# Kernel tuning notes

Measured on AMD Instinct MI355X. Metric: run time of the kernel, lower is better.

## Reference

```python
import jax, jax.numpy as jnp
import numpy as np

M_SQRT1_2 = 0.7071067811865476
P_DROP = 0.1  # activation_dropout


def setup_inputs() -> dict:
    key = jax.random.key(0)
    k1, k2, k3, k4 = jax.random.split(key, 4)
    N, FFN, EMB = 8192, 4096, 1024
    x = jax.random.normal(k1, (N, FFN), dtype=jnp.float16)
    weight = (jax.random.normal(k2, (EMB, FFN), dtype=jnp.float32) * (1.0 / np.sqrt(FFN))).astype(jnp.float16)
    bias = jax.random.normal(k3, (EMB,), dtype=jnp.float16)
    mask = jax.random.uniform(k4, (N, FFN)) >= P_DROP  # keep mask (bool)
    return {"x": x, "weight": weight, "bias": bias, "mask": mask}


def reference(x, weight, bias, mask):
    # GELU computed in fp32, cast back to fp16 (matches the custom IR)
    xf = x.astype(jnp.float32)
    g = (0.5 * xf * (1.0 + jax.lax.erf(xf * M_SQRT1_2))).astype(jnp.float16)
    # dropout: mask then scale by 1/(1-p) in fp16
    scale = jnp.float16(1.0 / (1.0 - P_DROP))
    h = g * mask.astype(jnp.float16) * scale  # [N, FFN]
    # y[N0, N2] = sum_N1 h[N0, N1] * weight[N2, N1] + bias[N2]
    y = jnp.einsum('nf,ef->ne', h, weight) + bias[None, :]
    return y
```

## Files before the change

kernel.cpp:

```cpp
#include <hip/hip_runtime.h>
#include <stdint.h>

typedef uint32_t u32;
typedef uint16_t u16;

static constexpr int M_DIM = 8192;
static constexpr int N_DIM = 1024;
static constexpr int K_DIM = 4096;

static constexpr int BM = 256;
static constexpr int BN = 128;
static constexpr int BK = 64;
static constexpr int KT64 = K_DIM / BK;
static constexpr int K_TILES32 = K_DIM / 32;
static constexpr int MB_TILES = M_DIM / 16;
static constexpr int NB_TILES = N_DIM / 16;

static constexpr size_t FRAG_U16 = 512;
static constexpr size_t HT_BYTES = (size_t)MB_TILES * K_TILES32 * FRAG_U16 * 2;
static constexpr size_t WT_BYTES = (size_t)NB_TILES * K_TILES32 * FRAG_U16 * 2;
static constexpr size_t WS_NEEDED = HT_BYTES + WT_BYTES;

typedef __attribute__((ext_vector_type(8))) _Float16 half8;
typedef __attribute__((ext_vector_type(4))) float f32x4;

__device__ __forceinline__ u32 pack2(float a, float b) {
  union { _Float16 h[2]; u32 u; } p;
  p.h[0] = (_Float16)a;
  p.h[1] = (_Float16)b;
  return p.u;
}

__device__ __forceinline__ float gelu_drop(float x, u32 keep) {
  float ax = fabsf(x);
  float z  = ax * 0.70710678f;
  float t  = __builtin_amdgcn_rcpf(fmaf(0.3275911f, z, 1.0f));
  float poly = fmaf(fmaf(fmaf(fmaf(1.061405429f, t, -1.453152027f),
                              t, 1.421413741f),
                         t, -0.284496736f),
                    t, 0.254829592f) * t;
  float e   = exp2f(z * z * -1.44269504f);
  float erf = fmaf(-poly, e, 1.0f);
  float g   = 0.5f * x * (1.0f + copysignf(erf, x));
  return keep ? g * 1.1111112f : 0.0f;
}

__device__ __forceinline__ void async_cp16(const void* g, void* l) {
  __builtin_amdgcn_global_load_lds((__attribute__((address_space(1))) u32*)g,
                                   (__attribute__((address_space(3))) u32*)l,
                                   16, 0, 0);
}

static constexpr int H_WAVES = MB_TILES * K_TILES32;
static constexpr int W_WAVES = NB_TILES * K_TILES32;
static constexpr int PACK_BLOCKS = (H_WAVES + W_WAVES) / 4;

__global__ __launch_bounds__(256)
void pack_kernel(const float* __restrict__ X, const int* __restrict__ Mask,
                 const float* __restrict__ W, u16* __restrict__ Ht, u16* __restrict__ Wt) {
  const int l     = threadIdx.x & 63;
  const int fi    = blockIdx.x * 4 + (threadIdx.x >> 6);
  const int row16 = l & 15;
  const int kof   = (l >> 4) << 3;

  if (fi < H_WAVES) {
    const int mb = fi >> 7, kt = fi & 127;
    const float* xp = X    + (size_t)(mb * 16 + row16) * K_DIM + kt * 32 + kof;
    const int*   mp = Mask + (size_t)(mb * 16 + row16) * K_DIM + kt * 32 + kof;
    float4 x0 = *(const float4*)(xp + 0);
    float4 x1 = *(const float4*)(xp + 4);
    uint4  m0 = *(const uint4*)(mp + 0);
    uint4  m1 = *(const uint4*)(mp + 4);
    u32 o0 = pack2(gelu_drop(x0.x, m0.x), gelu_drop(x0.y, m0.y));
    u32 o1 = pack2(gelu_drop(x0.z, m0.z), gelu_drop(x0.w, m0.w));
    u32 o2 = pack2(gelu_drop(x1.x, m1.x), gelu_drop(x1.y, m1.y));
    u32 o3 = pack2(gelu_drop(x1.z, m1.z), gelu_drop(x1.w, m1.w));
    *(uint4*)(Ht + (size_t)fi * FRAG_U16 + l * 8) = make_uint4(o0, o1, o2, o3);
  } else {
    const int fj = fi - H_WAVES;
    const int nb = fj >> 7, kt = fj & 127;
    const float* wp = W + (size_t)(nb * 16 + row16) * K_DIM + kt * 32 + kof;
    float4 w0 = *(const float4*)(wp + 0);
    float4 w1 = *(const float4*)(wp + 4);
    *(uint4*)(Wt + (size_t)fj * FRAG_U16 + l * 8) =
        make_uint4(pack2(w0.x, w0.y), pack2(w0.z, w0.w), pack2(w1.x, w1.y), pack2(w1.z, w1.w));
  }
}

__global__ __launch_bounds__(512, 1)
void gemm_kernel(const u16* __restrict__ Ht, const u16* __restrict__ Wt,
                 const float* __restrict__ Bias, float* __restrict__ Out) {
  __shared__ __attribute__((aligned(16))) u16 Abuf[2][BM * BK];
  __shared__ __attribute__((aligned(16))) u16 Bbuf[2][BN * BK];

  const int tid  = threadIdx.x;
  const int lane = tid & 63;
  const int wv   = tid >> 6;
  const int wr   = wv >> 1;
  const int wc   = wv & 1;

  const int bm = blockIdx.x & 31;
  const int bn = blockIdx.x >> 5;
  const int m0 = bm * BM;
  const int n0 = bn * BN;

  const char* aG = (const char*)Ht;
  const char* bG = (const char*)Wt;
  size_t aOff[4], bOff[2];
#pragma unroll
  for (int p = 0; p < 4; ++p) {
    const int s = tid + 512 * p, f = s >> 6;
    aOff[p] = ((size_t)(bm * 16 + (f >> 1)) * K_TILES32 + (f & 1)) * 1024 + (size_t)(s & 63) * 16;
  }
#pragma unroll
  for (int p = 0; p < 2; ++p) {
    const int s = tid + 512 * p, f = s >> 6;
    bOff[p] = ((size_t)(bn * 8 + (f >> 1)) * K_TILES32 + (f & 1)) * 1024 + (size_t)(s & 63) * 16;
  }

  auto stage = [&](int kt, int buf) {
    const size_t ko = (size_t)kt * 2048;
    char* ad = (char*)Abuf[buf];
    char* bd = (char*)Bbuf[buf];
#pragma unroll
    for (int p = 0; p < 4; ++p)
      async_cp16(aG + aOff[p] + ko, ad + (tid + 512 * p) * 16);
#pragma unroll
    for (int p = 0; p < 2; ++p)
      async_cp16(bG + bOff[p] + ko, bd + (tid + 512 * p) * 16);
  };

  f32x4 acc[4][4];
#pragma unroll
  for (int i = 0; i < 4; ++i)
#pragma unroll
    for (int j = 0; j < 4; ++j)
      acc[i][j] = (f32x4){0.f, 0.f, 0.f, 0.f};

  auto compute = [&](int buf) {
    const char* ab = (const char*)Abuf[buf];
    const char* bb = (const char*)Bbuf[buf];
#pragma unroll
    for (int kk = 0; kk < 2; ++kk) {
      half8 ar[4], br[4];
#pragma unroll
      for (int i = 0; i < 4; ++i)
        ar[i] = *(const half8*)(ab + (((wr * 4 + i) * 2 + kk) * 64 + lane) * 16);
#pragma unroll
      for (int j = 0; j < 4; ++j)
        br[j] = *(const half8*)(bb + (((wc * 4 + j) * 2 + kk) * 64 + lane) * 16);
#pragma unroll
      for (int i = 0; i < 4; ++i)
#pragma unroll
        for (int j = 0; j < 4; ++j)
          acc[i][j] = __builtin_amdgcn_mfma_f32_16x16x32_f16(ar[i], br[j], acc[i][j], 0, 0, 0);
    }
  };

  stage(0, 0);
  __syncthreads();

#pragma unroll 1
  for (int kt = 0; kt < KT64; kt += 2) {
    if (kt + 1 < KT64) stage(kt + 1, 1);
    compute(0);
    __syncthreads();
    if (kt + 2 < KT64) stage(kt + 2, 0);
    compute(1);
    __syncthreads();
  }

  const int fr = lane & 15;
  const int rq = (lane >> 4) << 2;
  float bv[4];
#pragma unroll
  for (int j = 0; j < 4; ++j)
    bv[j] = Bias[n0 + wc * 64 + j * 16 + fr];

#pragma unroll
  for (int i = 0; i < 4; ++i) {
    const int row0 = m0 + wr * 64 + i * 16 + rq;
#pragma unroll
    for (int j = 0; j < 4; ++j) {
      const int col = n0 + wc * 64 + j * 16 + fr;
#pragma unroll
      for (int r = 0; r < 4; ++r)
        Out[(size_t)(row0 + r) * N_DIM + col] = acc[i][j][r] + bv[j];
    }
  }
}

static constexpr int A_STRIDE = 40;

__global__ __launch_bounds__(256, 2)
void fused_fallback_kernel(const float* __restrict__ X, const float* __restrict__ W,
                           const float* __restrict__ Bias, const int* __restrict__ Mask,
                           float* __restrict__ Out) {
  __shared__ __attribute__((aligned(16))) _Float16 As[128 * A_STRIDE];
  __shared__ __attribute__((aligned(16))) _Float16 Bs[128 * 32];

  const int tid  = threadIdx.x;
  const int lane = tid & 63;
  const int wv   = tid >> 6;
  const int wr   = wv >> 1;
  const int wc   = wv & 1;
  const int bm = blockIdx.x & 63;
  const int bn = blockIdx.x >> 6;
  const int m0 = bm * 128;
  const int n0 = bn * 128;

  const int a_m = tid >> 1;
  const int a_k = (tid & 1) << 4;
  const float* xptr = X    + (size_t)(m0 + a_m) * K_DIM + a_k;
  const int*   mptr = Mask + (size_t)(m0 + a_m) * K_DIM + a_k;
  _Float16* a_lds = &As[a_m * A_STRIDE + a_k];

  const int i0 = tid, i1 = tid + 256;
  const float* wp0 = W + (size_t)(n0 + (i0 >> 2)) * K_DIM + ((i0 & 3) << 3);
  const float* wp1 = W + (size_t)(n0 + (i1 >> 2)) * K_DIM + ((i1 & 3) << 3);
  _Float16* bl0 = &Bs[i0 * 8];
  _Float16* bl1 = &Bs[i1 * 8];

  f32x4 acc[4][4];
#pragma unroll
  for (int i = 0; i < 4; ++i)
#pragma unroll
    for (int j = 0; j < 4; ++j)
      acc[i][j] = (f32x4){0.f, 0.f, 0.f, 0.f};

  float4 xf0 = *(const float4*)(xptr +  0);
  float4 xf1 = *(const float4*)(xptr +  4);
  float4 xf2 = *(const float4*)(xptr +  8);
  float4 xf3 = *(const float4*)(xptr + 12);
  uint4  mr0 = *(const uint4*)(mptr +  0);
  uint4  mr1 = *(const uint4*)(mptr +  4);
  uint4  mr2 = *(const uint4*)(mptr +  8);
  uint4  mr3 = *(const uint4*)(mptr + 12);
  float4 wf0 = *(const float4*)(wp0 + 0);
  float4 wf1 = *(const float4*)(wp0 + 4);
  float4 wf2 = *(const float4*)(wp1 + 0);
  float4 wf3 = *(const float4*)(wp1 + 4);

#pragma unroll 1
  for (int kt = 0; kt < 128; ++kt) {
    {
      float xs[16] = {xf0.x, xf0.y, xf0.z, xf0.w, xf1.x, xf1.y, xf1.z, xf1.w,
                      xf2.x, xf2.y, xf2.z, xf2.w, xf3.x, xf3.y, xf3.z, xf3.w};
      u32 mk[16]   = {mr0.x, mr0.y, mr0.z, mr0.w, mr1.x, mr1.y, mr1.z, mr1.w,
                      mr2.x, mr2.y, mr2.z, mr2.w, mr3.x, mr3.y, mr3.z, mr3.w};
      u32 ow[8];
#pragma unroll
      for (int e = 0; e < 8; ++e)
        ow[e] = pack2(gelu_drop(xs[2 * e], mk[2 * e]), gelu_drop(xs[2 * e + 1], mk[2 * e + 1]));
      ((uint4*)a_lds)[0] = make_uint4(ow[0], ow[1], ow[2], ow[3]);
      ((uint4*)a_lds)[1] = make_uint4(ow[4], ow[5], ow[6], ow[7]);
    }
    {
      *(uint4*)bl0 = make_uint4(pack2(wf0.x, wf0.y), pack2(wf0.z, wf0.w),
                                pack2(wf1.x, wf1.y), pack2(wf1.z, wf1.w));
      *(uint4*)bl1 = make_uint4(pack2(wf2.x, wf2.y), pack2(wf2.z, wf2.w),
                                pack2(wf3.x, wf3.y), pack2(wf3.z, wf3.w));
    }
    __syncthreads();

    if (kt + 1 < 128) {
      xptr += 32; mptr += 32; wp0 += 32; wp1 += 32;
      xf0 = *(const float4*)(xptr +  0);
      xf1 = *(const float4*)(xptr +  4);
      xf2 = *(const float4*)(xptr +  8);
      xf3 = *(const float4*)(xptr + 12);
      mr0 = *(const uint4*)(mptr +  0);
      mr1 = *(const uint4*)(mptr +  4);
      mr2 = *(const uint4*)(mptr +  8);
      mr3 = *(const uint4*)(mptr + 12);
      wf0 = *(const float4*)(wp0 + 0);
      wf1 = *(const float4*)(wp0 + 4);
      wf2 = *(const float4*)(wp1 + 0);
      wf3 = *(const float4*)(wp1 + 4);
    }

    {
      const int fr2 = lane & 15;
      const int fk2 = (lane >> 4) << 3;
      half8 ar[4], br[4];
#pragma unroll
      for (int i = 0; i < 4; ++i)
        ar[i] = *(const half8*)&As[(wr * 64 + i * 16 + fr2) * A_STRIDE + fk2];
#pragma unroll
      for (int j = 0; j < 4; ++j)
        br[j] = *(const half8*)&Bs[(wc * 64 + j * 16 + fr2) * 32 + fk2];
#pragma unroll
      for (int i = 0; i < 4; ++i)
#pragma unroll
        for (int j = 0; j < 4; ++j)
          acc[i][j] = __builtin_amdgcn_mfma_f32_16x16x32_f16(ar[i], br[j], acc[i][j], 0, 0, 0);
    }
    __syncthreads();
  }

  const int fr = lane & 15;
  const int rq = (lane >> 4) << 2;
  float bv[4];
#pragma unroll
  for (int j = 0; j < 4; ++j)
    bv[j] = Bias[n0 + wc * 64 + j * 16 + fr];
#pragma unroll
  for (int i = 0; i < 4; ++i) {
    const int row0 = m0 + wr * 64 + i * 16 + rq;
#pragma unroll
    for (int j = 0; j < 4; ++j) {
      const int col = n0 + wc * 64 + j * 16 + fr;
#pragma unroll
      for (int r = 0; r < 4; ++r)
        Out[(size_t)(row0 + r) * N_DIM + col] = acc[i][j][r] + bv[j];
    }
  }
}

extern "C" void kernel_launch(void* const* d_in, const int* in_sizes, int n_in,
                              void* d_out, int out_size, void* d_ws, size_t ws_size,
                              hipStream_t stream) {
  const float* X    = (const float*)d_in[0];
  const float* W    = (const float*)d_in[1];
  const float* Bias = (const float*)d_in[2];
  const int*   Mk   = (const int*)d_in[3];
  float* Out = (float*)d_out;

  if (ws_size >= WS_NEEDED) {
    u16* Ht = (u16*)d_ws;
    u16* Wt = (u16*)((char*)d_ws + HT_BYTES);
    pack_kernel<<<PACK_BLOCKS, 256, 0, stream>>>(X, Mk, W, Ht, Wt);
    gemm_kernel<<<(M_DIM / BM) * (N_DIM / BN), 512, 0, stream>>>(Ht, Wt, Bias, Out);
  } else {
    fused_fallback_kernel<<<64 * 8, 256, 0, stream>>>(X, W, Bias, Mk, Out);
  }
}
```

Baseline: 392.5 us.

## Triple-buffer GEMM LDS with vmcnt waits and widen pack to two fragments per wave

The GEMM main loop moves from double to triple LDS buffering. Loads are issued two K-tiles ahead, and each iteration uses one barrier guarded by a partial s_waitcnt vmcnt in place of __syncthreads. This is meant to hide global-to-LDS latency behind MFMA, and s_setprio raises wave priority around the MFMA bursts. The pack kernel now handles 16 contiguous K elements per lane, covering two fragments, so each lane issues wider loads and two stores. The cost is more LDS (three buffers of 48KB each, 144KB), and correctness depends on the hardcoded vmcnt(6) matching the number of loads per stage.

After: 401.2 us. 2.2% more time.

```diff
diff --git a/kernel.cpp b/kernel.cpp
--- a/kernel.cpp
+++ b/kernel.cpp
@@ -51,47 +51,68 @@
                                    16, 0, 0);
 }
 
-static constexpr int H_WAVES = MB_TILES * K_TILES32;
-static constexpr int W_WAVES = NB_TILES * K_TILES32;
-static constexpr int PACK_BLOCKS = (H_WAVES + W_WAVES) / 4;
+static constexpr int H_PAIRS = MB_TILES * (K_TILES32 / 2);
+static constexpr int W_PAIRS = NB_TILES * (K_TILES32 / 2);
+static constexpr int PACK_BLOCKS = (H_PAIRS + W_PAIRS) / 4;
 
 __global__ __launch_bounds__(256)
 void pack_kernel(const float* __restrict__ X, const int* __restrict__ Mask,
                  const float* __restrict__ W, u16* __restrict__ Ht, u16* __restrict__ Wt) {
   const int l     = threadIdx.x & 63;
-  const int fi    = blockIdx.x * 4 + (threadIdx.x >> 6);
+  const int pi    = blockIdx.x * 4 + (threadIdx.x >> 6);
   const int row16 = l & 15;
-  const int kof   = (l >> 4) << 3;
-
-  if (fi < H_WAVES) {
-    const int mb = fi >> 7, kt = fi & 127;
-    const float* xp = X    + (size_t)(mb * 16 + row16) * K_DIM + kt * 32 + kof;
-    const int*   mp = Mask + (size_t)(mb * 16 + row16) * K_DIM + kt * 32 + kof;
+  const int kof   = (l >> 4) << 4;
+
+  const int fsub = kof >> 5;
+  const int q0   = (kof & 31) >> 3;
+
+  if (pi < H_PAIRS) {
+    const int mb = pi >> 6, kp = pi & 63;
+    const size_t src = (size_t)(mb * 16 + row16) * K_DIM + kp * 64 + kof;
+    const float* xp = X    + src;
+    const int*   mp = Mask + src;
     float4 x0 = *(const float4*)(xp + 0);
     float4 x1 = *(const float4*)(xp + 4);
+    float4 x2 = *(const float4*)(xp + 8);
+    float4 x3 = *(const float4*)(xp + 12);
     uint4  m0 = *(const uint4*)(mp + 0);
     uint4  m1 = *(const uint4*)(mp + 4);
+    uint4  m2 = *(const uint4*)(mp + 8);
+    uint4  m3 = *(const uint4*)(mp + 12);
     u32 o0 = pack2(gelu_drop(x0.x, m0.x), gelu_drop(x0.y, m0.y));
     u32 o1 = pack2(gelu_drop(x0.z, m0.z), gelu_drop(x0.w, m0.w));
     u32 o2 = pack2(gelu_drop(x1.x, m1.x), gelu_drop(x1.y, m1.y));
     u32 o3 = pack2(gelu_drop(x1.z, m1.z), gelu_drop(x1.w, m1.w));
-    *(uint4*)(Ht + (size_t)fi * FRAG_U16 + l * 8) = make_uint4(o0, o1, o2, o3);
+    u32 o4 = pack2(gelu_drop(x2.x, m2.x), gelu_drop(x2.y, m2.y));
+    u32 o5 = pack2(gelu_drop(x2.z, m2.z), gelu_drop(x2.w, m2.w));
+    u32 o6 = pack2(gelu_drop(x3.x, m3.x), gelu_drop(x3.y, m3.y));
+    u32 o7 = pack2(gelu_drop(x3.z, m3.z), gelu_drop(x3.w, m3.w));
+    const int f = kp * 2 + fsub;
+    u16* dst = Ht + (size_t)(mb * 128 + f) * FRAG_U16 + (size_t)(row16 + 16 * q0) * 8;
+    *(uint4*)(dst)       = make_uint4(o0, o1, o2, o3);
+    *(uint4*)(dst + 128) = make_uint4(o4, o5, o6, o7);
   } else {
-    const int fj = fi - H_WAVES;
-    const int nb = fj >> 7, kt = fj & 127;
-    const float* wp = W + (size_t)(nb * 16 + row16) * K_DIM + kt * 32 + kof;
+    const int pj = pi - H_PAIRS;
+    const int nb = pj >> 6, kp = pj & 63;
+    const float* wp = W + (size_t)(nb * 16 + row16) * K_DIM + kp * 64 + kof;
     float4 w0 = *(const float4*)(wp + 0);
     float4 w1 = *(const float4*)(wp + 4);
-    *(uint4*)(Wt + (size_t)fj * FRAG_U16 + l * 8) =
-        make_uint4(pack2(w0.x, w0.y), pack2(w0.z, w0.w), pack2(w1.x, w1.y), pack2(w1.z, w1.w));
+    float4 w2 = *(const float4*)(wp + 8);
+    float4 w3 = *(const float4*)(wp + 12);
+    const int f = kp * 2 + fsub;
+    u16* dst = Wt + (size_t)(nb * 128 + f) * FRAG_U16 + (size_t)(row16 + 16 * q0) * 8;
+    *(uint4*)(dst)       = make_uint4(pack2(w0.x, w0.y), pack2(w0.z, w0.w),
+                                      pack2(w1.x, w1.y), pack2(w1.z, w1.w));
+    *(uint4*)(dst + 128) = make_uint4(pack2(w2.x, w2.y), pack2(w2.z, w2.w),
+                                      pack2(w3.x, w3.y), pack2(w3.z, w3.w));
   }
 }
 
 __global__ __launch_bounds__(512, 1)
 void gemm_kernel(const u16* __restrict__ Ht, const u16* __restrict__ Wt,
                  const float* __restrict__ Bias, float* __restrict__ Out) {
-  __shared__ __attribute__((aligned(16))) u16 Abuf[2][BM * BK];
-  __shared__ __attribute__((aligned(16))) u16 Bbuf[2][BN * BK];
+  __shared__ __attribute__((aligned(16))) u16 Abuf[3][BM * BK];
+  __shared__ __attribute__((aligned(16))) u16 Bbuf[3][BN * BK];
 
   const int tid  = threadIdx.x;
   const int lane = tid & 63;
@@ -149,25 +170,38 @@
 #pragma unroll
       for (int j = 0; j < 4; ++j)
         br[j] = *(const half8*)(bb + (((wc * 4 + j) * 2 + kk) * 64 + lane) * 16);
+      __builtin_amdgcn_s_setprio(1);
 #pragma unroll
       for (int i = 0; i < 4; ++i)
 #pragma unroll
         for (int j = 0; j < 4; ++j)
           acc[i][j] = __builtin_amdgcn_mfma_f32_16x16x32_f16(ar[i], br[j], acc[i][j], 0, 0, 0);
+      __builtin_amdgcn_s_setprio(0);
     }
   };
 
   stage(0, 0);
-  __syncthreads();
-
+  stage(1, 1);
+
+  int cur = 0;
 #pragma unroll 1
-  for (int kt = 0; kt < KT64; kt += 2) {
-    if (kt + 1 < KT64) stage(kt + 1, 1);
-    compute(0);
-    __syncthreads();
-    if (kt + 2 < KT64) stage(kt + 2, 0);
-    compute(1);
-    __syncthreads();
+  for (int kt = 0; kt < KT64; ++kt) {
+    if (kt + 2 < KT64) {
+      asm volatile("s_waitcnt vmcnt(6)" ::: "memory");
+      __builtin_amdgcn_s_barrier();
+      asm volatile("" ::: "memory");
+      stage(kt + 2, cur == 0 ? 2 : cur - 1);
+    } else if (kt + 1 < KT64) {
+      asm volatile("s_waitcnt vmcnt(6)" ::: "memory");
+      __builtin_amdgcn_s_barrier();
+      asm volatile("" ::: "memory");
+    } else {
+      asm volatile("s_waitcnt vmcnt(0)" ::: "memory");
+      __builtin_amdgcn_s_barrier();
+      asm volatile("" ::: "memory");
+    }
+    compute(cur);
+    cur = (cur == 2) ? 0 : cur + 1;
   }
 
   const int fr = lane & 15;
```

## Use row-major H with XOR-swizzled LDS, smaller 128x128 tiles, streaming pack

Applied to the files above, without the earlier changes.

The GELU/dropout pack now writes H row-major with fully coalesced 16-element-per-thread streaming loads, software-pipelined across four iterations, instead of fragment-tiled. W is still packed in MFMA fragment order. The GEMM moves from 256x128 tiles with 512 threads and a double-buffered LDS to 128x128 tiles with 256 threads, two blocks per CU and a single LDS buffer. A tiles are read from LDS through an XOR swizzle to avoid bank conflicts. Dropping the double buffer exposes load latency, which the second resident block is expected to hide.

After: 416.3 us. 1.06x slower.

```diff
diff --git a/kernel.cpp b/kernel.cpp
--- a/kernel.cpp
+++ b/kernel.cpp
@@ -8,18 +8,10 @@
 static constexpr int N_DIM = 1024;
 static constexpr int K_DIM = 4096;
 
-static constexpr int BM = 256;
-static constexpr int BN = 128;
-static constexpr int BK = 64;
-static constexpr int KT64 = K_DIM / BK;
-static constexpr int K_TILES32 = K_DIM / 32;
-static constexpr int MB_TILES = M_DIM / 16;
-static constexpr int NB_TILES = N_DIM / 16;
-
+static constexpr size_t H_BYTES  = (size_t)M_DIM * K_DIM * 2;
 static constexpr size_t FRAG_U16 = 512;
-static constexpr size_t HT_BYTES = (size_t)MB_TILES * K_TILES32 * FRAG_U16 * 2;
-static constexpr size_t WT_BYTES = (size_t)NB_TILES * K_TILES32 * FRAG_U16 * 2;
-static constexpr size_t WS_NEEDED = HT_BYTES + WT_BYTES;
+static constexpr size_t WT_BYTES = 64ull * 128 * FRAG_U16 * 2;
+static constexpr size_t WS_NEEDED = H_BYTES + WT_BYTES;
 
 typedef __attribute__((ext_vector_type(8))) _Float16 half8;
 typedef __attribute__((ext_vector_type(4))) float f32x4;
@@ -51,47 +43,102 @@
                                    16, 0, 0);
 }
 
-static constexpr int H_WAVES = MB_TILES * K_TILES32;
-static constexpr int W_WAVES = NB_TILES * K_TILES32;
-static constexpr int PACK_BLOCKS = (H_WAVES + W_WAVES) / 4;
+static constexpr int W_PAIRS = 64 * 64;
+static constexpr int WPACK_BLOCKS = W_PAIRS / 4;
+static constexpr int PACKX_BLOCKS = 2048;
+static constexpr size_t PACK_STR = 2048ull * 256 * 16;
 
 __global__ __launch_bounds__(256)
 void pack_kernel(const float* __restrict__ X, const int* __restrict__ Mask,
-                 const float* __restrict__ W, u16* __restrict__ Ht, u16* __restrict__ Wt) {
-  const int l     = threadIdx.x & 63;
-  const int fi    = blockIdx.x * 4 + (threadIdx.x >> 6);
-  const int row16 = l & 15;
-  const int kof   = (l >> 4) << 3;
-
-  if (fi < H_WAVES) {
-    const int mb = fi >> 7, kt = fi & 127;
-    const float* xp = X    + (size_t)(mb * 16 + row16) * K_DIM + kt * 32 + kof;
-    const int*   mp = Mask + (size_t)(mb * 16 + row16) * K_DIM + kt * 32 + kof;
-    float4 x0 = *(const float4*)(xp + 0);
-    float4 x1 = *(const float4*)(xp + 4);
-    uint4  m0 = *(const uint4*)(mp + 0);
-    uint4  m1 = *(const uint4*)(mp + 4);
-    u32 o0 = pack2(gelu_drop(x0.x, m0.x), gelu_drop(x0.y, m0.y));
-    u32 o1 = pack2(gelu_drop(x0.z, m0.z), gelu_drop(x0.w, m0.w));
-    u32 o2 = pack2(gelu_drop(x1.x, m1.x), gelu_drop(x1.y, m1.y));
-    u32 o3 = pack2(gelu_drop(x1.z, m1.z), gelu_drop(x1.w, m1.w));
-    *(uint4*)(Ht + (size_t)fi * FRAG_U16 + l * 8) = make_uint4(o0, o1, o2, o3);
-  } else {
-    const int fj = fi - H_WAVES;
-    const int nb = fj >> 7, kt = fj & 127;
-    const float* wp = W + (size_t)(nb * 16 + row16) * K_DIM + kt * 32 + kof;
+                 const float* __restrict__ W, u16* __restrict__ H, u16* __restrict__ Wt) {
+  if (blockIdx.x < WPACK_BLOCKS) {
+    const int l     = threadIdx.x & 63;
+    const int pj    = blockIdx.x * 4 + (threadIdx.x >> 6);
+    const int row16 = l & 15;
+    const int kof   = (l >> 4) << 4;
+    const int fsub  = kof >> 5;
+    const int q0    = (kof & 31) >> 3;
+    const int nb = pj >> 6, kp = pj & 63;
+    const float* wp = W + (size_t)(nb * 16 + row16) * K_DIM + kp * 64 + kof;
     float4 w0 = *(const float4*)(wp + 0);
     float4 w1 = *(const float4*)(wp + 4);
-    *(uint4*)(Wt + (size_t)fj * FRAG_U16 + l * 8) =
-        make_uint4(pack2(w0.x, w0.y), pack2(w0.z, w0.w), pack2(w1.x, w1.y), pack2(w1.z, w1.w));
-  }
-}
-
-__global__ __launch_bounds__(512, 1)
-void gemm_kernel(const u16* __restrict__ Ht, const u16* __restrict__ Wt,
+    float4 w2 = *(const float4*)(wp + 8);
+    float4 w3 = *(const float4*)(wp + 12);
+    const int f = kp * 2 + fsub;
+    u16* dst = Wt + (size_t)(nb * 128 + f) * FRAG_U16 + (size_t)(row16 + 16 * q0) * 8;
+    *(uint4*)(dst)       = make_uint4(pack2(w0.x, w0.y), pack2(w0.z, w0.w),
+                                      pack2(w1.x, w1.y), pack2(w1.z, w1.w));
+    *(uint4*)(dst + 128) = make_uint4(pack2(w2.x, w2.y), pack2(w2.z, w2.w),
+                                      pack2(w3.x, w3.y), pack2(w3.z, w3.w));
+    return;
+  }
+
+  const u32 t = (blockIdx.x - WPACK_BLOCKS) * 256 + threadIdx.x;
+  const float* xb = X    + (size_t)t * 16;
+  const int*   mb = Mask + (size_t)t * 16;
+  u16*         hb = H    + (size_t)t * 16;
+
+  float4 xA0, xA1, xA2, xA3, xB0, xB1, xB2, xB3;
+  uint4  mA0, mA1, mA2, mA3, mB0, mB1, mB2, mB3;
+
+  auto loadA = [&](int it) {
+    const float* p = xb + (size_t)it * PACK_STR;
+    const int*   q = mb + (size_t)it * PACK_STR;
+    xA0 = *(const float4*)(p + 0);  xA1 = *(const float4*)(p + 4);
+    xA2 = *(const float4*)(p + 8);  xA3 = *(const float4*)(p + 12);
+    mA0 = *(const uint4*)(q + 0);   mA1 = *(const uint4*)(q + 4);
+    mA2 = *(const uint4*)(q + 8);   mA3 = *(const uint4*)(q + 12);
+  };
+  auto loadB = [&](int it) {
+    const float* p = xb + (size_t)it * PACK_STR;
+    const int*   q = mb + (size_t)it * PACK_STR;
+    xB0 = *(const float4*)(p + 0);  xB1 = *(const float4*)(p + 4);
+    xB2 = *(const float4*)(p + 8);  xB3 = *(const float4*)(p + 12);
+    mB0 = *(const uint4*)(q + 0);   mB1 = *(const uint4*)(q + 4);
+    mB2 = *(const uint4*)(q + 8);   mB3 = *(const uint4*)(q + 12);
+  };
+  auto procA = [&](int it) {
+    u16* d = hb + (size_t)it * PACK_STR;
+    *(uint4*)(d + 0) = make_uint4(
+        pack2(gelu_drop(xA0.x, mA0.x), gelu_drop(xA0.y, mA0.y)),
+        pack2(gelu_drop(xA0.z, mA0.z), gelu_drop(xA0.w, mA0.w)),
+        pack2(gelu_drop(xA1.x, mA1.x), gelu_drop(xA1.y, mA1.y)),
+        pack2(gelu_drop(xA1.z, mA1.z), gelu_drop(xA1.w, mA1.w)));
+    *(uint4*)(d + 8) = make_uint4(
+        pack2(gelu_drop(xA2.x, mA2.x), gelu_drop(xA2.y, mA2.y)),
+        pack2(gelu_drop(xA2.z, mA2.z), gelu_drop(xA2.w, mA2.w)),
+        pack2(gelu_drop(xA3.x, mA3.x), gelu_drop(xA3.y, mA3.y)),
+        pack2(gelu_drop(xA3.z, mA3.z), gelu_drop(xA3.w, mA3.w)));
+  };
+  auto procB = [&](int it) {
+    u16* d = hb + (size_t)it * PACK_STR;
+    *(uint4*)(d + 0) = make_uint4(
+        pack2(gelu_drop(xB0.x, mB0.x), gelu_drop(xB0.y, mB0.y)),
+        pack2(gelu_drop(xB0.z, mB0.z), gelu_drop(xB0.w, mB0.w)),
+        pack2(gelu_drop(xB1.x, mB1.x), gelu_drop(xB1.y, mB1.y)),
+        pack2(gelu_drop(xB1.z, mB1.z), gelu_drop(xB1.w, mB1.w)));
+    *(uint4*)(d + 8) = make_uint4(
+        pack2(gelu_drop(xB2.x, mB2.x), gelu_drop(xB2.y, mB2.y)),
+        pack2(gelu_drop(xB2.z, mB2.z), gelu_drop(xB2.w, mB2.w)),
+        pack2(gelu_drop(xB3.x, mB3.x), gelu_drop(xB3.y, mB3.y)),
+        pack2(gelu_drop(xB3.z, mB3.z), gelu_drop(xB3.w, mB3.w)));
+  };
+
+  loadA(0);
+  loadB(1);
+  procA(0);
+  loadA(2);
+  procB(1);
+  loadB(3);
+  procA(2);
+  procB(3);
+}
+
+__global__ __launch_bounds__(256, 2)
+void gemm_kernel(const u16* __restrict__ H, const u16* __restrict__ Wt,
                  const float* __restrict__ Bias, float* __restrict__ Out) {
-  __shared__ __attribute__((aligned(16))) u16 Abuf[2][BM * BK];
-  __shared__ __attribute__((aligned(16))) u16 Bbuf[2][BN * BK];
+  __shared__ __attribute__((aligned(16))) u16 Asl[8192];
+  __shared__ __attribute__((aligned(16))) u16 Bsl[8192];
 
   const int tid  = threadIdx.x;
   const int lane = tid & 63;
@@ -99,36 +146,23 @@
   const int wr   = wv >> 1;
   const int wc   = wv & 1;
 
-  const int bm = blockIdx.x & 31;
-  const int bn = blockIdx.x >> 5;
-  const int m0 = bm * BM;
-  const int n0 = bn * BN;
-
-  const char* aG = (const char*)Ht;
-  const char* bG = (const char*)Wt;
-  size_t aOff[4], bOff[2];
+  const int bn = blockIdx.x & 7;
+  const int bm = blockIdx.x >> 3;
+  const int m0 = bm * 128;
+  const int n0 = bn * 128;
+
+  const char* Hc = (const char*)H;
+  const char* Wc = (const char*)Wt;
+
+  size_t aSrc[4], bSrc[4];
 #pragma unroll
   for (int p = 0; p < 4; ++p) {
-    const int s = tid + 512 * p, f = s >> 6;
-    aOff[p] = ((size_t)(bm * 16 + (f >> 1)) * K_TILES32 + (f & 1)) * 1024 + (size_t)(s & 63) * 16;
-  }
-#pragma unroll
-  for (int p = 0; p < 2; ++p) {
-    const int s = tid + 512 * p, f = s >> 6;
-    bOff[p] = ((size_t)(bn * 8 + (f >> 1)) * K_TILES32 + (f & 1)) * 1024 + (size_t)(s & 63) * 16;
-  }
-
-  auto stage = [&](int kt, int buf) {
-    const size_t ko = (size_t)kt * 2048;
-    char* ad = (char*)Abuf[buf];
-    char* bd = (char*)Bbuf[buf];
-#pragma unroll
-    for (int p = 0; p < 4; ++p)
-      async_cp16(aG + aOff[p] + ko, ad + (tid + 512 * p) * 16);
-#pragma unroll
-    for (int p = 0; p < 2; ++p)
-      async_cp16(bG + bOff[p] + ko, bd + (tid + 512 * p) * 16);
-  };
+    const int s = tid + 256 * p;
+    const int row = s >> 3, ch = s & 7;
+    aSrc[p] = (size_t)(m0 + row) * (K_DIM * 2) + (size_t)(((u32)ch ^ ((u32)row & 7u)) * 16);
+    const int f = s >> 6;
+    bSrc[p] = ((size_t)((bn * 8 + (f >> 1)) * 128 + (f & 1))) * 1024 + (size_t)(s & 63) * 16;
+  }
 
   f32x4 acc[4][4];
 #pragma unroll
@@ -137,36 +171,38 @@
     for (int j = 0; j < 4; ++j)
       acc[i][j] = (f32x4){0.f, 0.f, 0.f, 0.f};
 
-  auto compute = [&](int buf) {
-    const char* ab = (const char*)Abuf[buf];
-    const char* bb = (const char*)Bbuf[buf];
+#pragma unroll 1
+  for (int ks = 0; ks < 64; ++ks) {
+    const size_t ka = (size_t)ks * 128;
+    const size_t kb = (size_t)ks * 2048;
+#pragma unroll
+    for (int p = 0; p < 4; ++p)
+      async_cp16(Hc + aSrc[p] + ka, (char*)Asl + (size_t)(tid + 256 * p) * 16);
+#pragma unroll
+    for (int p = 0; p < 4; ++p)
+      async_cp16(Wc + bSrc[p] + kb, (char*)Bsl + (size_t)(tid + 256 * p) * 16);
+    __syncthreads();
+
+    const char* ac = (const char*)Asl;
+    const char* bc = (const char*)Bsl;
 #pragma unroll
     for (int kk = 0; kk < 2; ++kk) {
       half8 ar[4], br[4];
 #pragma unroll
-      for (int i = 0; i < 4; ++i)
-        ar[i] = *(const half8*)(ab + (((wr * 4 + i) * 2 + kk) * 64 + lane) * 16);
+      for (int i = 0; i < 4; ++i) {
+        const int row = wr * 64 + i * 16 + (lane & 15);
+        const u32 ch = ((u32)(kk * 4 + (lane >> 4))) ^ ((u32)lane & 7u);
+        ar[i] = *(const half8*)(ac + (size_t)row * 128 + ch * 16);
+      }
 #pragma unroll
       for (int j = 0; j < 4; ++j)
-        br[j] = *(const half8*)(bb + (((wc * 4 + j) * 2 + kk) * 64 + lane) * 16);
+        br[j] = *(const half8*)(bc + (size_t)(((wc * 4 + j) * 2 + kk) * 1024) + lane * 16);
 #pragma unroll
       for (int i = 0; i < 4; ++i)
 #pragma unroll
         for (int j = 0; j < 4; ++j)
           acc[i][j] = __builtin_amdgcn_mfma_f32_16x16x32_f16(ar[i], br[j], acc[i][j], 0, 0, 0);
     }
-  };
-
-  stage(0, 0);
-  __syncthreads();
-
-#pragma unroll 1
-  for (int kt = 0; kt < KT64; kt += 2) {
-    if (kt + 1 < KT64) stage(kt + 1, 1);
-    compute(0);
-    __syncthreads();
-    if (kt + 2 < KT64) stage(kt + 2, 0);
-    compute(1);
     __syncthreads();
   }
 
@@ -176,7 +212,6 @@
 #pragma unroll
   for (int j = 0; j < 4; ++j)
     bv[j] = Bias[n0 + wc * 64 + j * 16 + fr];
-
 #pragma unroll
   for (int i = 0; i < 4; ++i) {
     const int row0 = m0 + wr * 64 + i * 16 + rq;
@@ -327,10 +362,10 @@
   float* Out = (float*)d_out;
 
   if (ws_size >= WS_NEEDED) {
-    u16* Ht = (u16*)d_ws;
-    u16* Wt = (u16*)((char*)d_ws + HT_BYTES);
-    pack_kernel<<<PACK_BLOCKS, 256, 0, stream>>>(X, Mk, W, Ht, Wt);
-    gemm_kernel<<<(M_DIM / BM) * (N_DIM / BN), 512, 0, stream>>>(Ht, Wt, Bias, Out);
+    u16* H  = (u16*)d_ws;
+    u16* Wt = (u16*)((char*)d_ws + H_BYTES);
+    pack_kernel<<<WPACK_BLOCKS + PACKX_BLOCKS, 256, 0, stream>>>(X, Mk, W, H, Wt);
+    gemm_kernel<<<(M_DIM / 128) * (N_DIM / 128), 256, 0, stream>>>(H, Wt, Bias, Out);
   } else {
     fused_fallback_kernel<<<64 * 8, 256, 0, stream>>>(X, W, Bias, Mk, Out);
   }
```
